# Optimization experiments

Hardware: AMD Instinct MI355X
Metric: run time of the kernel (lower is better)

## Reference

```python
import jax, jax.numpy as jnp
import numpy as np

B, S, E, H = 1, 2048, 1024, 16
D = E // H          # head_dim = 64
SM_SCALE = 0.5      # module default, not 1/sqrt(D)


def setup_inputs() -> dict:
    key = jax.random.key(0)
    ks = jax.random.split(key, 9)
    std = 0.02
    return {
        "x":  jax.random.normal(ks[0], (B, S, E), dtype=jnp.float32),
        "Wq": jax.random.normal(ks[1], (E, E), dtype=jnp.float32) * std,
        "bq": jnp.zeros((E,), dtype=jnp.float32),
        "Wk": jax.random.normal(ks[2], (E, E), dtype=jnp.float32) * std,
        "bk": jnp.zeros((E,), dtype=jnp.float32),
        "Wv": jax.random.normal(ks[3], (E, E), dtype=jnp.float32) * std,
        "bv": jnp.zeros((E,), dtype=jnp.float32),
        "Wo": jax.random.normal(ks[4], (E, E), dtype=jnp.float32) * std,
        "bo": jnp.zeros((E,), dtype=jnp.float32),
    }


def _split_heads(t):
    # [B,S,E] -> [B,H,S,D]
    b, s, _ = t.shape
    return jnp.transpose(t.reshape(b, s, H, D), (0, 2, 1, 3))


def reference(x, Wq, bq, Wk, bk, Wv, bv, Wo, bo):
    # Projections in fp32, then cast to bf16 (matches module's .astype(bf16))
    q = _split_heads((x @ Wq + bq).astype(jnp.bfloat16))
    k = _split_heads((x @ Wk + bk).astype(jnp.bfloat16))
    v = _split_heads((x @ Wv + bv).astype(jnp.bfloat16))

    # Blockwise loop in the original is mathematically full causal attention
    scores = jnp.einsum("bhqd,bhkd->bhqk", q, k) * SM_SCALE  # [B,H,S,S] bf16
    causal = jnp.tril(jnp.ones((S, S), dtype=bool))
    scores = jnp.where(causal[None, None, :, :], scores, -jnp.inf)
    probs = jax.nn.softmax(scores, axis=-1)
    out = jnp.einsum("bhqk,bhkd->bhqd", probs, v)            # [B,H,S,D]

    out = jnp.transpose(out, (0, 2, 1, 3)).reshape(B, S, E)
    # dropout off (is_training=False / rate=0); final projection in fp32
    return out.astype(jnp.float32) @ Wo + bo
```

## Files before the change

### kernel.cpp

```cpp
#include <hip/hip_runtime.h>
#include <hip/hip_bf16.h>

#define S_LEN 2048
#define E_DIM 1024
#define NH    16
#define HD    64
#define SM_SCALE 0.5f

typedef short bf16x8_t  __attribute__((ext_vector_type(8)));
typedef float f32x4_t   __attribute__((ext_vector_type(4)));
typedef float f32x16_t  __attribute__((ext_vector_type(16)));
typedef __bf16 bf16x4_t __attribute__((ext_vector_type(4)));

static __device__ __forceinline__ unsigned short f2bf_bits(float f) {
    return __builtin_bit_cast(unsigned short, (__bf16)f);
}

#define GLD16(gp, lp) __builtin_amdgcn_global_load_lds(                       \
    (const __attribute__((address_space(1))) void*)(gp),                      \
    (__attribute__((address_space(3))) void*)(lp), 16, 0, 0)

__global__ void k_prep(const float* __restrict__ x,
                       const float* __restrict__ Wq, const float* __restrict__ Wk,
                       const float* __restrict__ Wv, const float* __restrict__ Wo,
                       __bf16* __restrict__ xb, __bf16* __restrict__ wt) {
    const int z = blockIdx.z;
    if (z < 4) {
        __shared__ float tile[32][33];
        const float* W = z == 0 ? Wq : z == 1 ? Wk : z == 2 ? Wv : Wo;
        __bf16* o = wt + (size_t)z * E_DIM * E_DIM;
        const int tx = threadIdx.x, ty = threadIdx.y;
        const int bx = blockIdx.x * 32, by = blockIdx.y * 32;
#pragma unroll
        for (int j = 0; j < 32; j += 8)
            tile[ty + j][tx] = W[(size_t)(by + ty + j) * E_DIM + bx + tx];
        __syncthreads();
#pragma unroll
        for (int j = 0; j < 32; j += 8)
            o[(size_t)(bx + ty + j) * E_DIM + by + tx] = (__bf16)tile[tx][ty + j];
    } else {
        const int bid = (z - 4) * 1024 + blockIdx.y * 32 + blockIdx.x;
        const int tid = threadIdx.y * 32 + threadIdx.x;
        const int i = bid * 256 + tid;
        const float4 v = ((const float4*)x)[i];
        bf16x4_t o4;
        o4.x = (__bf16)v.x; o4.y = (__bf16)v.y; o4.z = (__bf16)v.z; o4.w = (__bf16)v.w;
        ((bf16x4_t*)xb)[i] = o4;
    }
}

__global__ __launch_bounds__(256) void k_gemm_qkv(
    const __bf16* __restrict__ xb, const __bf16* __restrict__ wt,
    const float* __restrict__ bq, const float* __restrict__ bk, const float* __restrict__ bv,
    __bf16* __restrict__ qkv) {
    __shared__ __align__(16) unsigned short As[2][128 * 32];
    __shared__ __align__(16) unsigned short Bs[2][128 * 32];

    const int z = blockIdx.z;
    const __bf16* Bt = wt + (size_t)z * E_DIM * E_DIM;
    const float* bias = z == 0 ? bq : z == 1 ? bk : bv;
    __bf16* out = qkv + (size_t)z * NH * S_LEN * HD;

    const int tid = threadIdx.x, w = tid >> 6, l = tid & 63;
    const int lm = l & 15, q4 = l >> 4;
    const int bm = blockIdx.y, bn = blockIdx.x;
    const int wm = w >> 1, wn = w & 1;

    const int sm = (w << 4) + (l >> 2);
    const int skk = (l & 3) << 3;
    const __bf16* Ag = xb + (size_t)(bm * 128 + sm) * E_DIM + skk;
    const __bf16* Bg = Bt + (size_t)(bn * 128 + sm) * E_DIM + skk;
    const int woff = w << 9;

    f32x4_t acc[4][4];
#pragma unroll
    for (int i = 0; i < 4; i++)
#pragma unroll
        for (int j = 0; j < 4; j++) { acc[i][j].x = 0.f; acc[i][j].y = 0.f; acc[i][j].z = 0.f; acc[i][j].w = 0.f; }

    GLD16(Ag, &As[0][woff]);
    GLD16(Ag + (size_t)64 * E_DIM, &As[0][woff + 2048]);
    GLD16(Bg, &Bs[0][woff]);
    GLD16(Bg + (size_t)64 * E_DIM, &Bs[0][woff + 2048]);
    __syncthreads();

    for (int s = 0; s < 32; s++) {
        const int bb = s & 1;
        if (s < 31) {
            const int k0 = (s + 1) * 32;
            GLD16(Ag + k0, &As[bb ^ 1][woff]);
            GLD16(Ag + (size_t)64 * E_DIM + k0, &As[bb ^ 1][woff + 2048]);
            GLD16(Bg + k0, &Bs[bb ^ 1][woff]);
            GLD16(Bg + (size_t)64 * E_DIM + k0, &Bs[bb ^ 1][woff + 2048]);
        }

        bf16x8_t af[4], bfr[4];
#pragma unroll
        for (int mt = 0; mt < 4; mt++)
            af[mt] = *(const bf16x8_t*)&As[bb][(wm * 64 + mt * 16 + lm) * 32 + q4 * 8];
#pragma unroll
        for (int nt = 0; nt < 4; nt++)
            bfr[nt] = *(const bf16x8_t*)&Bs[bb][(wn * 64 + nt * 16 + lm) * 32 + q4 * 8];
#pragma unroll
        for (int mt = 0; mt < 4; mt++)
#pragma unroll
            for (int nt = 0; nt < 4; nt++)
                acc[mt][nt] = __builtin_amdgcn_mfma_f32_16x16x32_bf16(af[mt], bfr[nt], acc[mt][nt], 0, 0, 0);
        __syncthreads();
    }

#pragma unroll
    for (int nt = 0; nt < 4; nt++) {
        const int n = bn * 128 + wn * 64 + nt * 16 + lm;
        const float bval = bias[n];
        const int h = n >> 6, d = n & 63;
        const int tile0 = bm * 2 + wm;
        if (z == 2) {
            const int db = d >> 5, dl = d & 31;
#pragma unroll
            for (int mt = 0; mt < 4; mt++) {
                __bf16* ob = out + (((size_t)h * 32 + tile0) * 8 + db * 4 + mt) * 512
                                 + (dl + (q4 >> 1) * 32) * 8 + (q4 & 1) * 4;
                union { unsigned short s4[4]; uint2 u; } pk;
#pragma unroll
                for (int i = 0; i < 4; i++) pk.s4[i] = f2bf_bits(acc[mt][nt][i] + bval);
                *(uint2*)ob = pk.u;
            }
        } else {
            const float scale = (z == 0) ? SM_SCALE : 1.0f;
            const int kc = d >> 4, khalf = (d >> 3) & 1, j = d & 7;
#pragma unroll
            for (int mt = 0; mt < 4; mt++) {
                __bf16* ob = out + (((size_t)h * 32 + tile0) * 8 + (mt >> 1) * 4 + kc) * 512
                                 + ((mt & 1) * 16 + q4 * 4 + khalf * 32) * 8 + j;
#pragma unroll
                for (int i = 0; i < 4; i++)
                    ob[i * 8] = (__bf16)((acc[mt][nt][i] + bval) * scale);
            }
        }
    }
}

__global__ __launch_bounds__(256, 2) void k_attn(
    const __bf16* __restrict__ Qf, const __bf16* __restrict__ Kf, const __bf16* __restrict__ Vf,
    __bf16* __restrict__ attn) {
    __shared__ __align__(16) unsigned short KVs[2][2][4096];
    __shared__ __align__(16) unsigned short Pl[4][32 * 40];

    const int b = blockIdx.x;
    const int pi = b >> 4, h = b & 15;

    const int tid = threadIdx.x, w = tid >> 6, l = tid & 63;
    const int rh = w & 1, kh = w >> 1;
    const int l31 = l & 31, lh = l >> 5;

    const __bf16* Kb = Kf + (size_t)h * 32 * 4096;
    const __bf16* Vb = Vf + (size_t)h * 32 * 4096;

    unsigned short* Pw = Pl[w];

#pragma unroll
    for (int job = 0; job < 2; job++) {
        const int qt = job ? (31 - pi) : pi;
        const __bf16* Qb = Qf + ((size_t)h * 32 + qt) * 4096;

        bf16x8_t qf[4];
#pragma unroll
        for (int kc = 0; kc < 4; kc++)
            qf[kc] = *(const bf16x8_t*)(Qb + ((rh * 4 + kc) << 9) + l * 8);

        float lacc = 0.f;
        f32x16_t oacc[2];
#pragma unroll
        for (int db = 0; db < 2; db++)
#pragma unroll
            for (int r = 0; r < 16; r++) oacc[db][r] = 0.f;

        GLD16(Kb + (w << 9) + l * 8,       &KVs[0][0][(w << 9) + l * 8]);
        GLD16(Kb + ((w + 4) << 9) + l * 8, &KVs[0][0][((w + 4) << 9) + l * 8]);
        GLD16(Vb + (w << 9) + l * 8,       &KVs[0][1][(w << 9) + l * 8]);
        GLD16(Vb + ((w + 4) << 9) + l * 8, &KVs[0][1][((w + 4) << 9) + l * 8]);
        __syncthreads();

        for (int s = 0; s <= qt; s++) {
            const int bb = s & 1;
            if (s < qt) {
                const __bf16* Kg = Kb + (size_t)(s + 1) * 4096;
                const __bf16* Vg = Vb + (size_t)(s + 1) * 4096;
                GLD16(Kg + (w << 9) + l * 8,       &KVs[bb ^ 1][0][(w << 9) + l * 8]);
                GLD16(Kg + ((w + 4) << 9) + l * 8, &KVs[bb ^ 1][0][((w + 4) << 9) + l * 8]);
                GLD16(Vg + (w << 9) + l * 8,       &KVs[bb ^ 1][1][(w << 9) + l * 8]);
                GLD16(Vg + ((w + 4) << 9) + l * 8, &KVs[bb ^ 1][1][((w + 4) << 9) + l * 8]);
            }

            const bool diag = (s == qt);
            if (!(diag && kh > rh)) {
                f32x16_t st;
#pragma unroll
                for (int r = 0; r < 16; r++) st[r] = 0.f;
#pragma unroll
                for (int kc = 0; kc < 4; kc++) {
                    bf16x8_t kf = *(const bf16x8_t*)&KVs[bb][0][((kh * 4 + kc) << 9) + l * 8];
                    st = __builtin_amdgcn_mfma_f32_32x32x16_bf16(kf, qf[kc], st, 0, 0, 0);
                }
                if (diag && kh == rh) {
#pragma unroll
                    for (int r = 0; r < 16; r++) {
                        const int keyl = (r & 3) + 8 * (r >> 2) + 4 * lh;
                        st[r] = (keyl > l31) ? 0.f : __expf(st[r]);
                    }
                } else {
#pragma unroll
                    for (int r = 0; r < 16; r++) st[r] = __expf(st[r]);
                }
#pragma unroll
                for (int r = 0; r < 16; r++) lacc += st[r];
#pragma unroll
                for (int a = 0; a < 4; a++) {
                    union { unsigned short s4[4]; uint2 u; } pk;
#pragma unroll
                    for (int i = 0; i < 4; i++) pk.s4[i] = f2bf_bits(st[a * 4 + i]);
                    *(uint2*)&Pw[l31 * 40 + lh * 4 + a * 8] = pk.u;
                }
#pragma unroll
                for (int c = 0; c < 2; c++) {
                    bf16x8_t pf = *(const bf16x8_t*)&Pw[l31 * 40 + c * 16 + lh * 8];
#pragma unroll
                    for (int db = 0; db < 2; db++) {
                        bf16x8_t vf = *(const bf16x8_t*)&KVs[bb][1][((db * 4 + kh * 2 + c) << 9) + l * 8];
                        oacc[db] = __builtin_amdgcn_mfma_f32_32x32x16_bf16(vf, pf, oacc[db], 0, 0, 0);
                    }
                }
            }
            __syncthreads();
        }

        float* Ex = (float*)KVs;
        if (kh == 1) {
            float* e = Ex + (rh * 64 + l) * 34;
#pragma unroll
            for (int db = 0; db < 2; db++)
#pragma unroll
                for (int r = 0; r < 16; r++) e[db * 16 + r] = oacc[db][r];
            e[32] = lacc;
        }
        __syncthreads();
        if (kh == 0) {
            const float* e = Ex + (rh * 64 + l) * 34;
#pragma unroll
            for (int db = 0; db < 2; db++)
#pragma unroll
                for (int r = 0; r < 16; r++) oacc[db][r] += e[db * 16 + r];
            lacc += e[32];
            lacc += __shfl_xor(lacc, 32, 64);
            const float rl = 1.f / lacc;
            const int row = qt * 64 + rh * 32 + l31;
#pragma unroll
            for (int db = 0; db < 2; db++)
#pragma unroll
                for (int a = 0; a < 4; a++) {
                    union { unsigned short s4[4]; uint2 u; } pk;
#pragma unroll
                    for (int i = 0; i < 4; i++) pk.s4[i] = f2bf_bits(oacc[db][a * 4 + i] * rl);
                    *(uint2*)(attn + (size_t)row * E_DIM + h * HD + db * 32 + a * 8 + lh * 4) = pk.u;
                }
        }
        __syncthreads();
    }
}

__global__ __launch_bounds__(256) void k_gemm_out(
    const __bf16* __restrict__ A, const __bf16* __restrict__ Bt,
    const float* __restrict__ bias, float* __restrict__ out) {
    __shared__ __align__(16) unsigned short As[2][64 * 32];
    __shared__ __align__(16) unsigned short Bs[2][128 * 32];

    const int tid = threadIdx.x, w = tid >> 6, l = tid & 63;
    const int lm = l & 15, q4 = l >> 4;
    const int bm = blockIdx.y, bn = blockIdx.x;
    const int wm = w >> 1, wn = w & 1;

    const int sm = (w << 4) + (l >> 2);
    const int skk = (l & 3) << 3;
    const __bf16* Ag = A + (size_t)(bm * 64 + sm) * E_DIM + skk;
    const __bf16* Bg = Bt + (size_t)(bn * 128 + sm) * E_DIM + skk;
    const int woff = w << 9;

    f32x4_t acc[2][4];
#pragma unroll
    for (int i = 0; i < 2; i++)
#pragma unroll
        for (int j = 0; j < 4; j++) { acc[i][j].x = 0.f; acc[i][j].y = 0.f; acc[i][j].z = 0.f; acc[i][j].w = 0.f; }

    GLD16(Ag, &As[0][woff]);
    GLD16(Bg, &Bs[0][woff]);
    GLD16(Bg + (size_t)64 * E_DIM, &Bs[0][woff + 2048]);
    __syncthreads();

    for (int s = 0; s < 32; s++) {
        const int bb = s & 1;
        if (s < 31) {
            const int k0 = (s + 1) * 32;
            GLD16(Ag + k0, &As[bb ^ 1][woff]);
            GLD16(Bg + k0, &Bs[bb ^ 1][woff]);
            GLD16(Bg + (size_t)64 * E_DIM + k0, &Bs[bb ^ 1][woff + 2048]);
        }

        bf16x8_t af[2], bfr[4];
#pragma unroll
        for (int mt = 0; mt < 2; mt++)
            af[mt] = *(const bf16x8_t*)&As[bb][(wm * 32 + mt * 16 + lm) * 32 + q4 * 8];
#pragma unroll
        for (int nt = 0; nt < 4; nt++)
            bfr[nt] = *(const bf16x8_t*)&Bs[bb][(wn * 64 + nt * 16 + lm) * 32 + q4 * 8];
#pragma unroll
        for (int mt = 0; mt < 2; mt++)
#pragma unroll
            for (int nt = 0; nt < 4; nt++)
                acc[mt][nt] = __builtin_amdgcn_mfma_f32_16x16x32_bf16(af[mt], bfr[nt], acc[mt][nt], 0, 0, 0);
        __syncthreads();
    }

#pragma unroll
    for (int nt = 0; nt < 4; nt++) {
        const int n = bn * 128 + wn * 64 + nt * 16 + lm;
        const float bval = bias[n];
#pragma unroll
        for (int mt = 0; mt < 2; mt++) {
            const int r0 = bm * 64 + wm * 32 + mt * 16 + q4 * 4;
#pragma unroll
            for (int i = 0; i < 4; i++)
                out[(size_t)(r0 + i) * E_DIM + n] = acc[mt][nt][i] + bval;
        }
    }
}

extern "C" void kernel_launch(void* const* d_in, const int* in_sizes, int n_in,
                              void* d_out, int out_size, void* d_ws, size_t ws_size,
                              hipStream_t stream) {
    const float* x  = (const float*)d_in[0];
    const float* Wq = (const float*)d_in[1];
    const float* bq = (const float*)d_in[2];
    const float* Wk = (const float*)d_in[3];
    const float* bk = (const float*)d_in[4];
    const float* Wv = (const float*)d_in[5];
    const float* bv = (const float*)d_in[6];
    const float* Wo = (const float*)d_in[7];
    const float* bo = (const float*)d_in[8];
    float* out = (float*)d_out;

    char* ws = (char*)d_ws;
    __bf16* xb   = (__bf16*)(ws);
    __bf16* wt   = (__bf16*)(ws + ((size_t)4  << 20));
    __bf16* qkv  = (__bf16*)(ws + ((size_t)12 << 20));
    __bf16* attn = (__bf16*)(ws + ((size_t)24 << 20));

    k_prep<<<dim3(32, 32, 6), dim3(32, 8), 0, stream>>>(x, Wq, Wk, Wv, Wo, xb, wt);
    k_gemm_qkv<<<dim3(E_DIM / 128, S_LEN / 128, 3), 256, 0, stream>>>(xb, wt, bq, bk, bv, qkv);
    k_attn<<<dim3(256), 256, 0, stream>>>(
        qkv, qkv + (size_t)NH * S_LEN * HD, qkv + (size_t)2 * NH * S_LEN * HD, attn);
    k_gemm_out<<<dim3(E_DIM / 128, S_LEN / 64), 256, 0, stream>>>(
        attn, wt + (size_t)3 * E_DIM * E_DIM, bo, out);
}
```

Measured before the change: 158.1 us.

## Retile QKV GEMM as one fused 64x192 tile across Q/K/V weights

The QKV projection no longer launches three 128x128-tiled sub-GEMMs over blockIdx.z. It treats the three weight matrices as one 3072-wide N dimension with 64x192 block tiles on a 16x32 grid. Each wave now computes a 32x96 sub-tile and picks q/k/v, bias and output layout per column in the epilogue. The grid grows from 384 to 512 blocks, which should spread work more evenly across the CUs. In exchange, A-tile reuse drops because each block loads a smaller M slab while loading more B rows.

```diff
diff --git a/kernel.cpp b/kernel.cpp
--- a/kernel.cpp
+++ b/kernel.cpp
@@ -53,35 +53,30 @@
     const __bf16* __restrict__ xb, const __bf16* __restrict__ wt,
     const float* __restrict__ bq, const float* __restrict__ bk, const float* __restrict__ bv,
     __bf16* __restrict__ qkv) {
-    __shared__ __align__(16) unsigned short As[2][128 * 32];
-    __shared__ __align__(16) unsigned short Bs[2][128 * 32];
-
-    const int z = blockIdx.z;
-    const __bf16* Bt = wt + (size_t)z * E_DIM * E_DIM;
-    const float* bias = z == 0 ? bq : z == 1 ? bk : bv;
-    __bf16* out = qkv + (size_t)z * NH * S_LEN * HD;
+    __shared__ __align__(16) unsigned short As[2][64 * 32];
+    __shared__ __align__(16) unsigned short Bs[2][192 * 32];
 
     const int tid = threadIdx.x, w = tid >> 6, l = tid & 63;
     const int lm = l & 15, q4 = l >> 4;
-    const int bm = blockIdx.y, bn = blockIdx.x;
+    const int bn = blockIdx.x, bm = blockIdx.y;
     const int wm = w >> 1, wn = w & 1;
 
-    const int sm = (w << 4) + (l >> 2);
-    const int skk = (l & 3) << 3;
-    const __bf16* Ag = xb + (size_t)(bm * 128 + sm) * E_DIM + skk;
-    const __bf16* Bg = Bt + (size_t)(bn * 128 + sm) * E_DIM + skk;
+    const int sm = tid >> 2;
+    const int skk = (tid & 3) << 3;
+    const __bf16* Ag = xb + (size_t)(bm * 64 + sm) * E_DIM + skk;
+    const __bf16* Bg = wt + (size_t)(bn * 192 + sm) * E_DIM + skk;
     const int woff = w << 9;
 
-    f32x4_t acc[4][4];
-#pragma unroll
-    for (int i = 0; i < 4; i++)
-#pragma unroll
-        for (int j = 0; j < 4; j++) { acc[i][j].x = 0.f; acc[i][j].y = 0.f; acc[i][j].z = 0.f; acc[i][j].w = 0.f; }
+    f32x4_t acc[2][6];
+#pragma unroll
+    for (int i = 0; i < 2; i++)
+#pragma unroll
+        for (int j = 0; j < 6; j++) { acc[i][j].x = 0.f; acc[i][j].y = 0.f; acc[i][j].z = 0.f; acc[i][j].w = 0.f; }
 
     GLD16(Ag, &As[0][woff]);
-    GLD16(Ag + (size_t)64 * E_DIM, &As[0][woff + 2048]);
-    GLD16(Bg, &Bs[0][woff]);
-    GLD16(Bg + (size_t)64 * E_DIM, &Bs[0][woff + 2048]);
+#pragma unroll
+    for (int g = 0; g < 3; g++)
+        GLD16(Bg + (size_t)(g * 64) * E_DIM, &Bs[0][g * 2048 + woff]);
     __syncthreads();
 
     for (int s = 0; s < 32; s++) {
@@ -89,37 +84,38 @@
         if (s < 31) {
             const int k0 = (s + 1) * 32;
             GLD16(Ag + k0, &As[bb ^ 1][woff]);
-            GLD16(Ag + (size_t)64 * E_DIM + k0, &As[bb ^ 1][woff + 2048]);
-            GLD16(Bg + k0, &Bs[bb ^ 1][woff]);
-            GLD16(Bg + (size_t)64 * E_DIM + k0, &Bs[bb ^ 1][woff + 2048]);
-        }
-
-        bf16x8_t af[4], bfr[4];
-#pragma unroll
-        for (int mt = 0; mt < 4; mt++)
-            af[mt] = *(const bf16x8_t*)&As[bb][(wm * 64 + mt * 16 + lm) * 32 + q4 * 8];
-#pragma unroll
-        for (int nt = 0; nt < 4; nt++)
-            bfr[nt] = *(const bf16x8_t*)&Bs[bb][(wn * 64 + nt * 16 + lm) * 32 + q4 * 8];
-#pragma unroll
-        for (int mt = 0; mt < 4; mt++)
-#pragma unroll
-            for (int nt = 0; nt < 4; nt++)
+#pragma unroll
+            for (int g = 0; g < 3; g++)
+                GLD16(Bg + (size_t)(g * 64) * E_DIM + k0, &Bs[bb ^ 1][g * 2048 + woff]);
+        }
+
+        bf16x8_t af[2], bfr[6];
+#pragma unroll
+        for (int mt = 0; mt < 2; mt++)
+            af[mt] = *(const bf16x8_t*)&As[bb][(wm * 32 + mt * 16 + lm) * 32 + q4 * 8];
+#pragma unroll
+        for (int nt = 0; nt < 6; nt++)
+            bfr[nt] = *(const bf16x8_t*)&Bs[bb][(wn * 96 + nt * 16 + lm) * 32 + q4 * 8];
+#pragma unroll
+        for (int mt = 0; mt < 2; mt++)
+#pragma unroll
+            for (int nt = 0; nt < 6; nt++)
                 acc[mt][nt] = __builtin_amdgcn_mfma_f32_16x16x32_bf16(af[mt], bfr[nt], acc[mt][nt], 0, 0, 0);
         __syncthreads();
     }
 
 #pragma unroll
-    for (int nt = 0; nt < 4; nt++) {
-        const int n = bn * 128 + wn * 64 + nt * 16 + lm;
-        const float bval = bias[n];
-        const int h = n >> 6, d = n & 63;
-        const int tile0 = bm * 2 + wm;
+    for (int nt = 0; nt < 6; nt++) {
+        const int n = bn * 192 + wn * 96 + nt * 16 + lm;
+        const int z = n >> 10, n10 = n & 1023;
+        const float bval = (z == 0 ? bq : z == 1 ? bk : bv)[n10];
+        const int h = n10 >> 6, d = n10 & 63;
+        __bf16* out = qkv + (size_t)z * NH * S_LEN * HD;
         if (z == 2) {
             const int db = d >> 5, dl = d & 31;
 #pragma unroll
-            for (int mt = 0; mt < 4; mt++) {
-                __bf16* ob = out + (((size_t)h * 32 + tile0) * 8 + db * 4 + mt) * 512
+            for (int mt = 0; mt < 2; mt++) {
+                __bf16* ob = out + (((size_t)h * 32 + bm) * 8 + db * 4 + wm * 2 + mt) * 512
                                  + (dl + (q4 >> 1) * 32) * 8 + (q4 & 1) * 4;
                 union { unsigned short s4[4]; uint2 u; } pk;
 #pragma unroll
@@ -130,9 +126,9 @@
             const float scale = (z == 0) ? SM_SCALE : 1.0f;
             const int kc = d >> 4, khalf = (d >> 3) & 1, j = d & 7;
 #pragma unroll
-            for (int mt = 0; mt < 4; mt++) {
-                __bf16* ob = out + (((size_t)h * 32 + tile0) * 8 + (mt >> 1) * 4 + kc) * 512
-                                 + ((mt & 1) * 16 + q4 * 4 + khalf * 32) * 8 + j;
+            for (int mt = 0; mt < 2; mt++) {
+                __bf16* ob = out + (((size_t)h * 32 + bm) * 8 + wm * 4 + kc) * 512
+                                 + (mt * 16 + q4 * 4 + khalf * 32) * 8 + j;
 #pragma unroll
                 for (int i = 0; i < 4; i++)
                     ob[i * 8] = (__bf16)((acc[mt][nt][i] + bval) * scale);
@@ -356,7 +352,7 @@
     __bf16* attn = (__bf16*)(ws + ((size_t)24 << 20));
 
     k_prep<<<dim3(32, 32, 6), dim3(32, 8), 0, stream>>>(x, Wq, Wk, Wv, Wo, xb, wt);
-    k_gemm_qkv<<<dim3(E_DIM / 128, S_LEN / 128, 3), 256, 0, stream>>>(xb, wt, bq, bk, bv, qkv);
+    k_gemm_qkv<<<dim3(16, 32), 256, 0, stream>>>(xb, wt, bq, bk, bv, qkv);
     k_attn<<<dim3(256), 256, 0, stream>>>(
         qkv, qkv + (size_t)NH * S_LEN * HD, qkv + (size_t)2 * NH * S_LEN * HD, attn);
     k_gemm_out<<<dim3(E_DIM / 128, S_LEN / 64), 256, 0, stream>>>(
```

Result: no change. 157.9 us (-0.1%).
